# Kernel optimization log

Hardware: AMD Instinct MI355X
Metric: run time of the kernel (lower is better)

The kernel has to match this reference:

```python
import jax, jax.numpy as jnp
import numpy as np
from jax import lax

NAG = 3          # hardcoded in the torch module (query slices, catted_torches)
B = 4096         # batch_size per agent
H = 128          # hidden_dim
HEADS = 8
AD = H // HEADS  # attend_dim
STATE, ACT, SCAN = 48, 2, 256
OUTF, HID = 10, 256
NFEAT = 32 * (SCAN - 6)  # conv output features (two VALID convs: k5 then k3)
EPS = 1e-5

def leaky(x):
    return jnp.where(x >= 0, x, 0.01 * x)

def setup_inputs() -> dict:
    key = jax.random.key(0)
    ks = iter(jax.random.split(key, 40))
    def rn(shape, scale=0.05):
        return jax.random.normal(next(ks), shape, dtype=jnp.float32) * scale
    return {
        'obs':  jax.random.normal(next(ks), (NAG * B, STATE), jnp.float32),
        'acts': jax.random.normal(next(ks), (NAG * B, ACT), jnp.float32),
        'scan': jax.random.normal(next(ks), (NAG * B, SCAN), jnp.float32),
        'conv_w1': rn((32, 1, 5)),  'conv_b1': jnp.zeros((32,), jnp.float32),
        'conv_w2': rn((32, 32, 3)), 'conv_b2': jnp.zeros((32,), jnp.float32),
        'fc_w1': rn((256, NFEAT), 0.01), 'fc_b1': jnp.zeros((256,), jnp.float32),
        'fc_w2': rn((OUTF, 256)),        'fc_b2': jnp.zeros((OUTF,), jnp.float32),
        'enc_w': rn((H, STATE + ACT + OUTF)), 'enc_b': jnp.zeros((H,), jnp.float32),
        'Wk': rn((HEADS, AD, H)),
        'Wv': rn((HEADS, AD, H)), 'bv': jnp.zeros((HEADS, AD), jnp.float32),
        'Wq': rn((NAG, HEADS, AD, H)),
        'q1_w1': rn((HID, 2 * H)), 'q1_b1': jnp.zeros((HID,), jnp.float32),
        'q1_w2': rn((HID, HID)),   'q1_b2': jnp.zeros((HID,), jnp.float32),
        'q1_w3': rn((1, HID)),     'q1_b3': jnp.zeros((1,), jnp.float32),
        'q2_w1': rn((HID, 2 * H)), 'q2_b1': jnp.zeros((HID,), jnp.float32),
        'q2_w2': rn((HID, HID)),   'q2_b2': jnp.zeros((HID,), jnp.float32),
        'q2_w3': rn((1, HID)),     'q2_b3': jnp.zeros((1,), jnp.float32),
    }

def reference(obs, acts, scan, conv_w1, conv_b1, conv_w2, conv_b2,
              fc_w1, fc_b1, fc_w2, fc_b2, enc_w, enc_b, Wk, Wv, bv, Wq,
              q1_w1, q1_b1, q1_w2, q1_b2, q1_w3, q1_b3,
              q2_w1, q2_b1, q2_w2, q2_b2, q2_w3, q2_b3):
    dn = ('NCH', 'OIH', 'NCH')
    x = scan[:, None, :]                                            # [N,1,L]
    x = lax.conv_general_dilated(x, conv_w1, (1,), 'VALID', dimension_numbers=dn)
    x = jax.nn.relu(x + conv_b1[None, :, None])
    x = lax.conv_general_dilated(x, conv_w2, (1,), 'VALID', dimension_numbers=dn)
    x = jax.nn.relu(x + conv_b2[None, :, None])
    x = x.reshape(x.shape[0], -1)                                   # [N, NFEAT]
    x = jax.nn.relu(x @ fc_w1.T + fc_b1)
    feats = x @ fc_w2.T + fc_b2                                     # [N, OUTF]

    inps = jnp.concatenate([obs, acts, feats], axis=1)
    mu, var = inps.mean(0), inps.var(0)                             # BatchNorm1d (train, no affine)
    normed = (inps - mu) / jnp.sqrt(var + EPS)
    sa = leaky(normed @ enc_w.T + enc_b).reshape(NAG, B, H)         # [ag,B,H]

    keys = jnp.einsum('gbh,ndh->ngbd', sa, Wk)                      # [hd,ag,B,ad]
    vals = leaky(jnp.einsum('gbh,ndh->ngbd', sa, Wv) + bv[:, None, None, :])
    q = jnp.einsum('gbh,gndh->gnbd', sa, Wq)                        # [ag,hd,B,ad]

    logits = jnp.einsum('gnbd,nobd->gnbo', q, keys) / np.sqrt(AD)   # [ag,hd,B,ag]
    self_mask = jnp.eye(NAG, dtype=bool)[:, None, None, :]          # exclude own agent
    logits = jnp.where(self_mask, -jnp.inf, logits)
    w = jax.nn.softmax(logits, axis=-1)
    other = jnp.einsum('gnbo,nobd->gnbd', w, vals)                  # [ag,hd,B,ad]
    other = other.transpose(0, 2, 1, 3).reshape(NAG, B, H)          # heads concatenated

    emb = jnp.concatenate([sa, other], axis=2).reshape(NAG * B, 2 * H)

    def mlp(x, w1, b1, w2, b2, w3, b3):
        x = jax.nn.relu(x @ w1.T + b1)
        x = jax.nn.relu(x @ w2.T + b2)
        return x @ w3.T + b3

    q1 = mlp(emb, q1_w1, q1_b1, q1_w2, q1_b2, q1_w3, q1_b3)
    q2 = mlp(emb, q2_w1, q2_b1, q2_w2, q2_b2, q2_w3, q2_b3)
    return (q1, q2)
```

## Files before the change

### kernel.cpp

```cpp
#include <hip/hip_runtime.h>
#include <hip/hip_bf16.h>
#include <cstdint>
#include <cstddef>

typedef unsigned short u16;
typedef __attribute__((ext_vector_type(8))) __bf16 bf16x8;
typedef __attribute__((ext_vector_type(4))) float f32x4;

__device__ __forceinline__ u16 f2b(float f) {
  __hip_bfloat16 h = __float2bfloat16(f);
  return *reinterpret_cast<u16*>(&h);
}
__device__ __forceinline__ uint32_t pk2(float a, float b) {
  __hip_bfloat162 h = __float22bfloat162_rn(make_float2(a, b));
  return *reinterpret_cast<uint32_t*>(&h);
}
__device__ __forceinline__ float b2f(u16 u) {
  union { float f; uint32_t i; } x; x.i = ((uint32_t)u) << 16; return x.f;
}
__device__ __forceinline__ f32x4 mfma16(bf16x8 a, bf16x8 b, f32x4 c) {
  return __builtin_amdgcn_mfma_f32_16x16x32_bf16(a, b, c, 0, 0, 0);
}
__device__ __forceinline__ void async16(const void* g, void* l) {
  __builtin_amdgcn_global_load_lds((const __attribute__((address_space(1))) uint32_t*)g,
                                   (__attribute__((address_space(3))) uint32_t*)l, 16, 0, 0);
}

__global__ __launch_bounds__(256) void w1_perm(const float* __restrict__ w,
                                               u16* __restrict__ o) {
  __shared__ float L[8000];
  int j = blockIdx.x, tid = threadIdx.x;
  for (int i = tid; i < 8000; i += 256) L[i] = w[(size_t)j * 8000 + i];
  __syncthreads();
  for (int i = tid; i < 8000; i += 256) {
    int tt = i >> 5, cc = i & 31;
    int c2 = ((cc >> 2) & 1) * 16 + (cc >> 3) * 4 + (cc & 3);
    o[(size_t)j * 8000 + i] = f2b(L[c2 * 250 + tt]);
  }
}

struct CvtArgs {
  const float* src[13];
  void* dst[13];
  int cum[14];
  int kind[13];
};
__global__ __launch_bounds__(256) void f2b_multi(CvtArgs a, float* stats) {
  int i = blockIdx.x * 256 + threadIdx.x;
  if (blockIdx.x == 0 && threadIdx.x < 128) stats[threadIdx.x] = 0.f;
  int seg = 0;
  #pragma unroll
  for (int s = 1; s < 13; ++s) if (i >= a.cum[s]) seg = s;
  if (i < a.cum[13]) {
    int off = i - a.cum[seg];
    int kind = a.kind[seg];
    const float* src = a.src[seg];
    if (kind == 0) {
      ((u16*)a.dst[seg])[off] = f2b(src[off]);
    } else if (kind == 1) {
      int c2 = off / 96, rem = off - c2 * 96, kk = rem >> 5, c1 = rem & 31;
      ((u16*)a.dst[seg])[off] = f2b(src[(c2 * 32 + c1) * 3 + kk]);
    } else if (kind == 2) {
      int c1 = off >> 5, k = off & 31;
      ((u16*)a.dst[seg])[off] = f2b(k < 5 ? src[c1 * 5 + k] : 0.f);
    } else {
      ((float*)a.dst[seg])[off] = src[off];
    }
  }
}

__global__ __launch_bounds__(256) void conv_fused(
    const float* __restrict__ scan, const u16* __restrict__ w1g,
    const float* __restrict__ cb1, const u16* __restrict__ w2g,
    const float* __restrict__ cb2, u16* __restrict__ x) {
  __shared__ __align__(16) u16 A1[256 * 8];
  __shared__ __align__(16) u16 zbuf[4 * 8];
  __shared__ __align__(16) u16 h1T[258 * 40];
  int tid = threadIdx.x, lane = tid & 63, wv = tid >> 6;
  int l15 = lane & 15, quad = lane >> 4;
  const float* srow = scan + (size_t)blockIdx.x * 256;
  float sv[5];
  #pragma unroll
  for (int k = 0; k < 5; ++k) {
    int p = tid + k;
    sv[k] = (p < 256) ? srow[p] : 0.f;
  }
  union { bf16x8 v; uint32_t d[4]; } pk_;
  pk_.d[0] = pk2(sv[0], sv[1]);
  pk_.d[1] = pk2(sv[2], sv[3]);
  pk_.d[2] = pk2(sv[4], 0.f);
  pk_.d[3] = 0;
  *(bf16x8*)&A1[tid * 8] = pk_.v;
  if (lane < 8) zbuf[wv * 8 + lane] = 0;
  if (tid < 80) h1T[256 * 40 + tid] = 0;
  bf16x8 w1f[2];
  w1f[0] = *(const bf16x8*)&w1g[l15 * 32 + quad * 8];
  w1f[1] = *(const bf16x8*)&w1g[(16 + l15) * 32 + quad * 8];
  bf16x8 w2f[2][3];
  #pragma unroll
  for (int i = 0; i < 2; ++i)
    #pragma unroll
    for (int kk = 0; kk < 3; ++kk)
      w2f[i][kk] = *(const bf16x8*)&w2g[(i * 16 + l15) * 96 + kk * 32 + quad * 8];
  float cb1v[2][4], cb2v[2][4];
  #pragma unroll
  for (int i = 0; i < 2; ++i)
    #pragma unroll
    for (int r = 0; r < 4; ++r) {
      cb1v[i][r] = cb1[i * 16 + quad * 4 + r];
      cb2v[i][r] = cb2[i * 16 + quad * 4 + r];
    }
  asm volatile("s_waitcnt lgkmcnt(0)" ::: "memory");
  f32x4 zero = {0.f, 0.f, 0.f, 0.f};
  {
    f32x4 acc1[4][2];
    #pragma unroll
    for (int nt = 0; nt < 4; ++nt) { acc1[nt][0] = zero; acc1[nt][1] = zero; }
    #pragma unroll
    for (int nt = 0; nt < 4; ++nt) {
      int p = (wv * 4 + nt) * 16 + l15;
      const u16* bp = (quad == 0) ? &A1[p * 8] : &zbuf[wv * 8];
      bf16x8 bfr = *(const bf16x8*)bp;
      acc1[nt][0] = mfma16(w1f[0], bfr, acc1[nt][0]);
      acc1[nt][1] = mfma16(w1f[1], bfr, acc1[nt][1]);
    }
    #pragma unroll
    for (int nt = 0; nt < 4; ++nt) {
      int p = (wv * 4 + nt) * 16 + l15;
      #pragma unroll
      for (int mt = 0; mt < 2; ++mt) {
        float v0 = fmaxf(acc1[nt][mt][0] + cb1v[mt][0], 0.f);
        float v1 = fmaxf(acc1[nt][mt][1] + cb1v[mt][1], 0.f);
        float v2 = fmaxf(acc1[nt][mt][2] + cb1v[mt][2], 0.f);
        float v3 = fmaxf(acc1[nt][mt][3] + cb1v[mt][3], 0.f);
        uint2 u; u.x = pk2(v0, v1); u.y = pk2(v2, v3);
        *(uint2*)&h1T[p * 40 + mt * 16 + quad * 4] = u;
      }
    }
  }
  __syncthreads();
  f32x4 acc2[4][2];
  #pragma unroll
  for (int jj = 0; jj < 4; ++jj) { acc2[jj][0] = zero; acc2[jj][1] = zero; }
  #pragma unroll
  for (int kk = 0; kk < 3; ++kk) {
    #pragma unroll
    for (int jj = 0; jj < 4; ++jj) {
      int t = (wv * 4 + jj) * 16 + l15 + kk;
      bf16x8 h = *(const bf16x8*)&h1T[t * 40 + quad * 8];
      acc2[jj][0] = mfma16(w2f[0][kk], h, acc2[jj][0]);
      acc2[jj][1] = mfma16(w2f[1][kk], h, acc2[jj][1]);
    }
  }
  u16* xr = x + (size_t)blockIdx.x * 8000;
  #pragma unroll
  for (int jj = 0; jj < 4; ++jj) {
    int t = (wv * 4 + jj) * 16 + l15;
    if (t < 250) {
      union { bf16x8 v; uint32_t d[4]; } o_;
      #pragma unroll
      for (int i = 0; i < 2; ++i) {
        float v0 = fmaxf(acc2[jj][i][0] + cb2v[i][0], 0.f);
        float v1 = fmaxf(acc2[jj][i][1] + cb2v[i][1], 0.f);
        float v2 = fmaxf(acc2[jj][i][2] + cb2v[i][2], 0.f);
        float v3 = fmaxf(acc2[jj][i][3] + cb2v[i][3], 0.f);
        o_.d[i * 2]     = pk2(v0, v1);
        o_.d[i * 2 + 1] = pk2(v2, v3);
      }
      *(bf16x8*)&xr[t * 32 + quad * 8] = o_.v;
    }
  }
}

template <int MODE, int MROWS>
__global__ __launch_bounds__(256) void gemm_bt(
    const u16* __restrict__ A, int lda, const u16* __restrict__ W, int ldw,
    const float* __restrict__ bias, float* __restrict__ outF,
    u16* __restrict__ outB, int ldo, int nst, int a_sel, size_t out_zoff) {
  constexpr int AI = (MROWS * 8) / 256;
  __shared__ __align__(16) u16 As[2][MROWS * 64];
  __shared__ __align__(16) u16 Bs[2][128 * 64];
  int tid = threadIdx.x;
  int m0 = blockIdx.y * MROWS;
  int sel = (MODE == 4) ? blockIdx.x : 0;
  int n0 = (MODE == 4) ? 0 : blockIdx.x * 128;
  if (MODE == 4) {
    size_t woff = (sel < 2) ? (size_t)sel * 128 : (size_t)(256 + (m0 >> 12) * 128);
    W += woff * 128;
    outB += (size_t)sel * 12288 * 128;
  }
  if (a_sel) A += (size_t)(blockIdx.x >> 1) * a_sel;
  int kbase = blockIdx.z * nst * 64;
  if (MODE == 0) outF += (size_t)blockIdx.z * out_zoff;
  const u16* Ap = A + (size_t)m0 * lda + kbase;
  const u16* Wp = W + (size_t)n0 * ldw + kbase;
  int lane = tid & 63, wv = tid >> 6;
  int l15 = lane & 15, quad = lane >> 4;
  int wm = (wv >> 1) * (MROWS / 2), wn = (wv & 1) * 64;
  constexpr int MI = MROWS / 32;
  f32x4 zero = {0.f, 0.f, 0.f, 0.f};
  f32x4 acc[MI][4];
  #pragma unroll
  for (int i = 0; i < MI; ++i)
    #pragma unroll
    for (int j = 0; j < 4; ++j) acc[i][j] = zero;

  int sraA[AI], sofA[AI], sdsA[AI];
  #pragma unroll
  for (int it = 0; it < AI; ++it) {
    int c = it * 256 + tid;
    int row = c >> 3, slot = c & 7;
    sraA[it] = row;
    sofA[it] = ((slot ^ (row & 7)) * 8);
    sdsA[it] = c * 8;
  }
  int sraW[4], sofW[4], sdsW[4];
  #pragma unroll
  for (int it = 0; it < 4; ++it) {
    int c = it * 256 + tid;
    int row = c >> 3, slot = c & 7;
    sraW[it] = row;
    sofW[it] = ((slot ^ (row & 7)) * 8);
    sdsW[it] = c * 8;
  }
  int rslot[2];
  rslot[0] = ((quad ^ (l15 & 7)) * 8);
  rslot[1] = (((4 + quad) ^ (l15 & 7)) * 8);

  #pragma unroll 1
  for (int st = 0; st < nst; ++st) {
    if (st == 0) {
      #pragma unroll
      for (int it = 0; it < AI; ++it)
        async16(Ap + (size_t)sraA[it] * lda + sofA[it], &As[0][sdsA[it]]);
      #pragma unroll
      for (int it = 0; it < 4; ++it)
        async16(Wp + (size_t)sraW[it] * ldw + sofW[it], &Bs[0][sdsW[it]]);
    }
    __syncthreads();
    if (st + 1 < nst) {
      const u16* An = Ap + (st + 1) * 64;
      const u16* Wn = Wp + (st + 1) * 64;
      u16* Ad = &As[(st + 1) & 1][0];
      u16* Bd = &Bs[(st + 1) & 1][0];
      #pragma unroll
      for (int it = 0; it < AI; ++it)
        async16(An + (size_t)sraA[it] * lda + sofA[it], Ad + sdsA[it]);
      #pragma unroll
      for (int it = 0; it < 4; ++it)
        async16(Wn + (size_t)sraW[it] * ldw + sofW[it], Bd + sdsW[it]);
    }
    const u16* Ab = &As[st & 1][0];
    const u16* Bb = &Bs[st & 1][0];
    #pragma unroll
    for (int s = 0; s < 2; ++s) {
      bf16x8 af[MI], bfr[4];
      #pragma unroll
      for (int i = 0; i < MI; ++i)
        af[i] = *(const bf16x8*)&Ab[(wm + i * 16 + l15) * 64 + rslot[s]];
      #pragma unroll
      for (int j = 0; j < 4; ++j)
        bfr[j] = *(const bf16x8*)&Bb[(wn + j * 16 + l15) * 64 + rslot[s]];
      #pragma unroll
      for (int i = 0; i < MI; ++i)
        #pragma unroll
        for (int j = 0; j < 4; ++j) acc[i][j] = mfma16(af[i], bfr[j], acc[i][j]);
    }
  }
  #pragma unroll
  for (int i = 0; i < MI; ++i) {
    int mb = m0 + wm + i * 16 + quad * 4;
    #pragma unroll
    for (int j = 0; j < 4; ++j) {
      int n = n0 + wn + j * 16 + l15;
      float bv_ = (MODE == 1 || MODE == 4) ? bias[n] : 0.f;
      #pragma unroll
      for (int r = 0; r < 4; ++r) {
        float v = acc[i][j][r];
        if (MODE == 0) {
          outF[(size_t)(mb + r) * ldo + n] = v;
        } else if (MODE == 1) {
          v = fmaxf(v + bv_, 0.f);
          outB[(size_t)(mb + r) * ldo + n] = f2b(v);
        } else {
          if (sel == 1) { v += bv_; v = v >= 0.f ? v : 0.01f * v; }
          outB[(size_t)(mb + r) * ldo + n] = f2b(v);
        }
      }
    }
  }
}

__global__ __launch_bounds__(256) void fc2_stats(
    const float* __restrict__ hparts, const float* __restrict__ b1,
    const float* __restrict__ w2, const float* __restrict__ b2,
    const float* __restrict__ obs, const float* __restrict__ acts,
    float* __restrict__ inps, float* __restrict__ stats) {
  __shared__ float hL[32 * 260];
  __shared__ float w2L[10 * 260];
  __shared__ float b1L[256];
  __shared__ float ipL[32 * 61];
  int tid = threadIdx.x, r0 = blockIdx.x * 32;
  b1L[tid] = b1[tid];
  for (int i = tid; i < 2560; i += 256) w2L[(i >> 8) * 260 + (i & 255)] = w2[i];
  for (int i = tid; i < 32 * 48; i += 256) {
    int r = i / 48, f = i - r * 48;
    ipL[r * 61 + f] = obs[(size_t)(r0 + r) * 48 + f];
  }
  if (tid < 64) {
    int r = tid >> 1, f = tid & 1;
    ipL[r * 61 + 48 + f] = acts[(size_t)(r0 + r) * 2 + f];
  }
  __syncthreads();
  const size_t HS = (size_t)12288 * 256;
  for (int i = tid; i < 32 * 256; i += 256) {
    int r = i >> 8, c = i & 255;
    size_t g = (size_t)(r0 + r) * 256 + c;
    float v = b1L[c] + hparts[g] + hparts[g + HS] + hparts[g + 2 * HS] +
              hparts[g + 3 * HS] + hparts[g + 4 * HS];
    hL[r * 260 + c] = fmaxf(v, 0.f);
  }
  __syncthreads();
  {
    int r = tid >> 3, ob = tid & 7;
    for (int o = ob; o < 10; o += 8) {
      float a = 0.f;
      #pragma unroll 8
      for (int c = 0; c < 256; ++c) a += hL[r * 260 + c] * w2L[o * 260 + c];
      ipL[r * 61 + 50 + o] = a + b2[o];
    }
  }
  __syncthreads();
  for (int i = tid; i < 32 * 60; i += 256) {
    int r = i / 60, f = i - r * 60;
    inps[(size_t)(r0 + r) * 64 + f] = ipL[r * 61 + f];
  }
  if (tid < 60) {
    float s = 0.f, s2 = 0.f;
    for (int r = 0; r < 32; ++r) {
      float v = ipL[r * 61 + tid];
      s += v; s2 += v * v;
    }
    atomicAdd(&stats[tid], s);
    atomicAdd(&stats[64 + tid], s2);
  }
}

__global__ __launch_bounds__(256) void enc_kernel(
    const float* __restrict__ inps, const float* __restrict__ stats,
    const float* __restrict__ enc_w, const float* __restrict__ enc_b,
    u16* __restrict__ sab) {
  __shared__ float ewL[128 * 61];
  __shared__ float nrm[32 * 61];
  __shared__ float ebL[128];
  __shared__ float muL[60], ivL[60];
  int tid = threadIdx.x, r0 = blockIdx.x * 32;
  if (tid < 128) ebL[tid] = enc_b[tid];
  if (tid < 60) {
    float s = stats[tid], s2 = stats[64 + tid];
    float mu = s * (1.f / 12288.f);
    float var = s2 * (1.f / 12288.f) - mu * mu;
    muL[tid] = mu;
    ivL[tid] = rsqrtf(var + 1e-5f);
  }
  for (int i = tid; i < 128 * 60; i += 256) {
    int h = i / 60, f = i - h * 60;
    ewL[h * 61 + f] = enc_w[i];
  }
  __syncthreads();
  for (int i = tid; i < 32 * 60; i += 256) {
    int r = i / 60, f = i - r * 60;
    nrm[r * 61 + f] = (inps[(size_t)(r0 + r) * 64 + f] - muL[f]) * ivL[f];
  }
  __syncthreads();
  for (int i = tid; i < 32 * 128; i += 256) {
    int r = i >> 7, h = i & 127;
    float a = ebL[h];
    #pragma unroll 4
    for (int f = 0; f < 60; ++f) a += nrm[r * 61 + f] * ewL[h * 61 + f];
    a = a >= 0.f ? a : 0.01f * a;
    sab[(size_t)(r0 + r) * 128 + h] = f2b(a);
  }
}

__global__ __launch_bounds__(128) void attn_combine(
    const u16* __restrict__ qb, const u16* __restrict__ keysb,
    const u16* __restrict__ valsb, const u16* __restrict__ sab,
    u16* __restrict__ emb) {
  __shared__ float qL[3][128], kL[3][128], vL[3][128];
  __shared__ float lg[3][8][3], wgt[3][8][3];
  int b = blockIdx.x, t = threadIdx.x;
  #pragma unroll
  for (int o = 0; o < 3; ++o) {
    size_t base = (size_t)(o * 4096 + b) * 128 + t;
    qL[o][t] = b2f(qb[base]);
    kL[o][t] = b2f(keysb[base]);
    vL[o][t] = b2f(valsb[base]);
  }
  __syncthreads();
  if (t < 72) {
    int g = t / 24, n = (t / 3) % 8, o = t % 3;
    float a = 0.f;
    #pragma unroll
    for (int d = 0; d < 16; ++d) a += qL[g][n * 16 + d] * kL[o][n * 16 + d];
    lg[g][n][o] = (o == g) ? -1e30f : a * 0.25f;
  }
  __syncthreads();
  if (t < 24) {
    int g = t / 8, n = t % 8;
    float m = fmaxf(fmaxf(lg[g][n][0], lg[g][n][1]), lg[g][n][2]);
    float e0 = expf(lg[g][n][0] - m), e1 = expf(lg[g][n][1] - m),
          e2 = expf(lg[g][n][2] - m);
    float inv = 1.f / (e0 + e1 + e2);
    wgt[g][n][0] = e0 * inv; wgt[g][n][1] = e1 * inv; wgt[g][n][2] = e2 * inv;
  }
  __syncthreads();
  int n = t >> 4, d = t & 15;
  #pragma unroll
  for (int g = 0; g < 3; ++g) {
    float o_ = wgt[g][n][0] * vL[0][n * 16 + d] +
               wgt[g][n][1] * vL[1][n * 16 + d] +
               wgt[g][n][2] * vL[2][n * 16 + d];
    size_t rbase = (size_t)(g * 4096 + b) * 256;
    emb[rbase + 128 + t] = f2b(o_);
    emb[rbase + t] = sab[(size_t)(g * 4096 + b) * 128 + t];
  }
}

__global__ __launch_bounds__(256) void final_dot(
    const u16* __restrict__ t2ab, const float* __restrict__ w3a,
    const float* __restrict__ b3a, const float* __restrict__ w3b,
    const float* __restrict__ b3b, float* __restrict__ out) {
  int wv = threadIdx.x >> 6, lane = threadIdx.x & 63;
  int row = blockIdx.x * 4 + wv;
  float sa_ = 0.f, sb_ = 0.f;
  #pragma unroll
  for (int e = 0; e < 4; ++e) {
    int c = lane * 4 + e;
    sa_ += b2f(t2ab[(size_t)row * 512 + c]) * w3a[c];
    sb_ += b2f(t2ab[(size_t)row * 512 + 256 + c]) * w3b[c];
  }
  #pragma unroll
  for (int off = 32; off; off >>= 1) {
    sa_ += __shfl_down(sa_, off);
    sb_ += __shfl_down(sb_, off);
  }
  if (lane == 0) {
    out[row] = sa_ + b3a[0];
    out[12288 + row] = sb_ + b3b[0];
  }
}

extern "C" void kernel_launch(void* const* d_in, const int* in_sizes, int n_in,
                              void* d_out, int out_size, void* d_ws,
                              size_t ws_size, hipStream_t stream) {
  const float* obs  = (const float*)d_in[0];
  const float* acts = (const float*)d_in[1];
  const float* scan = (const float*)d_in[2];
  const float* cw1  = (const float*)d_in[3];
  const float* cb1  = (const float*)d_in[4];
  const float* cw2  = (const float*)d_in[5];
  const float* cb2  = (const float*)d_in[6];
  const float* fw1  = (const float*)d_in[7];
  const float* fb1  = (const float*)d_in[8];
  const float* fw2  = (const float*)d_in[9];
  const float* fb2  = (const float*)d_in[10];
  const float* encw = (const float*)d_in[11];
  const float* encb = (const float*)d_in[12];
  const float* Wk   = (const float*)d_in[13];
  const float* Wv   = (const float*)d_in[14];
  const float* bv   = (const float*)d_in[15];
  const float* Wq   = (const float*)d_in[16];
  const float* q1w1 = (const float*)d_in[17];
  const float* q1b1 = (const float*)d_in[18];
  const float* q1w2 = (const float*)d_in[19];
  const float* q1b2 = (const float*)d_in[20];
  const float* q1w3 = (const float*)d_in[21];
  const float* q1b3 = (const float*)d_in[22];
  const float* q2w1 = (const float*)d_in[23];
  const float* q2b1 = (const float*)d_in[24];
  const float* q2w2 = (const float*)d_in[25];
  const float* q2b2 = (const float*)d_in[26];
  const float* q2w3 = (const float*)d_in[27];
  const float* q2b3 = (const float*)d_in[28];
  float* out = (float*)d_out;
  char* ws = (char*)d_ws;
  if (ws_size < 264400000u) return;

  u16*   x     = (u16*)(ws + 0);
  u16*   w1b   = (u16*)(ws + 196608000);
  float* hpart = (float*)(ws + 200704000);
  float* stats = (float*)(ws + 263618560);
  u16*   wkvqb = (u16*)(ws + 263619584);
  u16*   m1ab  = (u16*)(ws + 263783424);
  u16*   m2ab  = (u16*)(ws + 264045568);
  u16*   w2g   = (u16*)(ws + 264307712);
  u16*   w1g   = (u16*)(ws + 264313856);
  float* bc1   = (float*)(ws + 264315904);
  float* bc2   = (float*)(ws + 264317952);
  float* inps  = (float*)(ws + 0);
  u16*   sab   = (u16*)(ws + 3145728);
  u16*   kvqb  = (u16*)(ws + 6291456);
  u16*   embb  = (u16*)(ws + 15728640);
  u16*   t1ab  = (u16*)(ws + 22020096);
  u16*   t2ab  = (u16*)(ws + 34603008);
  u16*   keysb = kvqb;
  u16*   valsb = kvqb + (size_t)12288 * 128;
  u16*   qb    = kvqb + (size_t)2 * 12288 * 128;

  w1_perm<<<256, 256, 0, stream>>>(fw1, w1b);
  CvtArgs ca;
  const float* srcs[13] = {Wk, Wv, Wq, q1w1, q2w1, q1w2, q2w2, cw2, cw1,
                           q1b1, q2b1, q1b2, q2b2};
  void* dsts[13] = {wkvqb, wkvqb + 16384, wkvqb + 32768, m1ab, m1ab + 65536,
                    m2ab, m2ab + 65536, w2g, w1g, bc1, bc1 + 256, bc2, bc2 + 256};
  const int sz[13] = {16384, 16384, 49152, 65536, 65536, 65536, 65536,
                      3072, 1024, 256, 256, 256, 256};
  const int kinds[13] = {0, 0, 0, 0, 0, 0, 0, 1, 2, 3, 3, 3, 3};
  int cum = 0;
  ca.cum[0] = 0;
  for (int i = 0; i < 13; ++i) {
    ca.src[i] = srcs[i]; ca.dst[i] = dsts[i]; ca.kind[i] = kinds[i];
    cum += sz[i]; ca.cum[i + 1] = cum;
  }
  f2b_multi<<<(cum + 255) / 256, 256, 0, stream>>>(ca, stats);

  conv_fused<<<12288, 256, 0, stream>>>(scan, w1g, cb1, w2g, cb2, x);
  gemm_bt<0, 64><<<dim3(2, 192, 5), 256, 0, stream>>>(
      x, 8000, w1b, 8000, nullptr, hpart, nullptr, 256, 25, 0,
      (size_t)12288 * 256);
  fc2_stats<<<384, 256, 0, stream>>>(hpart, fb1, fw2, fb2, obs, acts, inps, stats);
  enc_kernel<<<384, 256, 0, stream>>>(inps, stats, encw, encb, sab);
  gemm_bt<4, 64><<<dim3(3, 192, 1), 256, 0, stream>>>(
      sab, 128, wkvqb, 128, bv, nullptr, kvqb, 128, 2, 0, 0);
  attn_combine<<<4096, 128, 0, stream>>>(qb, keysb, valsb, sab, embb);
  gemm_bt<1, 64><<<dim3(4, 192, 1), 256, 0, stream>>>(
      embb, 256, m1ab, 256, bc1, nullptr, t1ab, 512, 4, 0, 0);
  gemm_bt<1, 64><<<dim3(4, 192, 1), 256, 0, stream>>>(
      t1ab, 512, m2ab, 256, bc2, nullptr, t2ab, 512, 4, 256, 0);
  final_dot<<<3072, 256, 0, stream>>>(t2ab, q1w3, q1b3, q2w3, q2b3, out);
}
```

Measured before the change: 364.3 us.

## Fuse conv stack into fc1 GEMM, streaming conv outputs through LDS

Replaces the separate conv kernel and split-K fc1 GEMM with one kernel. Each 512-thread block handles 64 rows: four waves compute the conv outputs one position at a time into a small LDS ring, and all eight waves consume them as K-slices of the fc1 GEMM, with double-buffered async weight loads. This removes the roughly 196MB bf16 intermediate and the split-K fp32 partial sums, and fc1 now writes a biased, ReLU'd bf16 output. The trade-off is only 192 blocks, a serial 250-step loop with a block barrier every step, and half the waves idle during the conv phase, so parallelism drops sharply.

Measured after the change: 430.5 us. 1.18x slower.

```diff
diff --git a/kernel.cpp b/kernel.cpp
--- a/kernel.cpp
+++ b/kernel.cpp
@@ -69,105 +69,176 @@
   }
 }
 
-__global__ __launch_bounds__(256) void conv_fused(
+__global__ __launch_bounds__(512) void mega(
     const float* __restrict__ scan, const u16* __restrict__ w1g,
     const float* __restrict__ cb1, const u16* __restrict__ w2g,
-    const float* __restrict__ cb2, u16* __restrict__ x) {
-  __shared__ __align__(16) u16 A1[256 * 8];
-  __shared__ __align__(16) u16 zbuf[4 * 8];
-  __shared__ __align__(16) u16 h1T[258 * 40];
+    const float* __restrict__ cb2, const u16* __restrict__ w1b,
+    const float* __restrict__ fb1, u16* __restrict__ hb) {
+  __shared__ __align__(16) u16 Ws[2][256 * 32];
+  __shared__ __align__(16) u16 Xs[2][64 * 40];
+  __shared__ __align__(16) u16 h1w[4][16 * 136];
   int tid = threadIdx.x, lane = tid & 63, wv = tid >> 6;
   int l15 = lane & 15, quad = lane >> 4;
-  const float* srow = scan + (size_t)blockIdx.x * 256;
-  float sv[5];
-  #pragma unroll
-  for (int k = 0; k < 5; ++k) {
-    int p = tid + k;
-    sv[k] = (p < 256) ? srow[p] : 0.f;
-  }
-  union { bf16x8 v; uint32_t d[4]; } pk_;
-  pk_.d[0] = pk2(sv[0], sv[1]);
-  pk_.d[1] = pk2(sv[2], sv[3]);
-  pk_.d[2] = pk2(sv[4], 0.f);
-  pk_.d[3] = 0;
-  *(bf16x8*)&A1[tid * 8] = pk_.v;
-  if (lane < 8) zbuf[wv * 8 + lane] = 0;
-  if (tid < 80) h1T[256 * 40 + tid] = 0;
-  bf16x8 w1f[2];
-  w1f[0] = *(const bf16x8*)&w1g[l15 * 32 + quad * 8];
-  w1f[1] = *(const bf16x8*)&w1g[(16 + l15) * 32 + quad * 8];
-  bf16x8 w2f[2][3];
-  #pragma unroll
-  for (int i = 0; i < 2; ++i)
-    #pragma unroll
-    for (int kk = 0; kk < 3; ++kk)
-      w2f[i][kk] = *(const bf16x8*)&w2g[(i * 16 + l15) * 96 + kk * 32 + quad * 8];
+  int r0 = blockIdx.x * 64;
+  f32x4 zero = {0.f, 0.f, 0.f, 0.f};
+  int wn = wv * 32;
+  f32x4 acc[4][2];
+  #pragma unroll
+  for (int i = 0; i < 4; ++i) { acc[i][0] = zero; acc[i][1] = zero; }
+  size_t wsrc[2]; int wdst[2];
+  #pragma unroll
+  for (int it = 0; it < 2; ++it) {
+    int c = it * 512 + tid;
+    int n = c >> 2, sl = c & 3;
+    int ks = sl ^ ((n >> 1) & 3);
+    wsrc[it] = (size_t)n * 8000 + ks * 8;
+    wdst[it] = c * 8;
+  }
+  int woff[2];
+  #pragma unroll
+  for (int j = 0; j < 2; ++j) {
+    int nj = wn + j * 16 + l15;
+    int sj = quad ^ ((nj >> 1) & 3);
+    woff[j] = nj * 32 + sj * 8;
+  }
+  int xoff[4];
+  #pragma unroll
+  for (int i = 0; i < 4; ++i) xoff[i] = (i * 16 + l15) * 40 + quad * 8;
+
+  bool cw = wv < 4;
+  const float* srow = scan + (size_t)(r0 + (wv & 3) * 16 + l15) * 256;
+  u16* myh1 = &h1w[wv & 3][0];
+  int h1wo = l15 * 136 + quad * 4;
+  int h1ro = l15 * 136 + quad * 8;
+  int xwo = ((wv & 3) * 16 + l15) * 40 + quad * 8;
+  bf16x8 w1f[2], w2f[2][3];
   float cb1v[2][4], cb2v[2][4];
-  #pragma unroll
-  for (int i = 0; i < 2; ++i)
-    #pragma unroll
-    for (int r = 0; r < 4; ++r) {
-      cb1v[i][r] = cb1[i * 16 + quad * 4 + r];
-      cb2v[i][r] = cb2[i * 16 + quad * 4 + r];
-    }
-  asm volatile("s_waitcnt lgkmcnt(0)" ::: "memory");
-  f32x4 zero = {0.f, 0.f, 0.f, 0.f};
-  {
-    f32x4 acc1[4][2];
-    #pragma unroll
-    for (int nt = 0; nt < 4; ++nt) { acc1[nt][0] = zero; acc1[nt][1] = zero; }
-    #pragma unroll
-    for (int nt = 0; nt < 4; ++nt) {
-      int p = (wv * 4 + nt) * 16 + l15;
-      const u16* bp = (quad == 0) ? &A1[p * 8] : &zbuf[wv * 8];
-      bf16x8 bfr = *(const bf16x8*)bp;
-      acc1[nt][0] = mfma16(w1f[0], bfr, acc1[nt][0]);
-      acc1[nt][1] = mfma16(w1f[1], bfr, acc1[nt][1]);
-    }
-    #pragma unroll
-    for (int nt = 0; nt < 4; ++nt) {
-      int p = (wv * 4 + nt) * 16 + l15;
-      #pragma unroll
-      for (int mt = 0; mt < 2; ++mt) {
-        float v0 = fmaxf(acc1[nt][mt][0] + cb1v[mt][0], 0.f);
-        float v1 = fmaxf(acc1[nt][mt][1] + cb1v[mt][1], 0.f);
-        float v2 = fmaxf(acc1[nt][mt][2] + cb1v[mt][2], 0.f);
-        float v3 = fmaxf(acc1[nt][mt][3] + cb1v[mt][3], 0.f);
-        uint2 u; u.x = pk2(v0, v1); u.y = pk2(v2, v3);
-        *(uint2*)&h1T[p * 40 + mt * 16 + quad * 4] = u;
+  if (cw) {
+    w1f[0] = *(const bf16x8*)&w1g[l15 * 32 + quad * 8];
+    w1f[1] = *(const bf16x8*)&w1g[(16 + l15) * 32 + quad * 8];
+    #pragma unroll
+    for (int i = 0; i < 2; ++i)
+      #pragma unroll
+      for (int kk = 0; kk < 3; ++kk)
+        w2f[i][kk] = *(const bf16x8*)&w2g[(i * 16 + l15) * 96 + kk * 32 + quad * 8];
+    #pragma unroll
+    for (int i = 0; i < 2; ++i)
+      #pragma unroll
+      for (int r = 0; r < 4; ++r) {
+        cb1v[i][r] = cb1[i * 16 + quad * 4 + r];
+        cb2v[i][r] = cb2[i * 16 + quad * 4 + r];
       }
-    }
-  }
-  __syncthreads();
-  f32x4 acc2[4][2];
-  #pragma unroll
-  for (int jj = 0; jj < 4; ++jj) { acc2[jj][0] = zero; acc2[jj][1] = zero; }
-  #pragma unroll
-  for (int kk = 0; kk < 3; ++kk) {
-    #pragma unroll
-    for (int jj = 0; jj < 4; ++jj) {
-      int t = (wv * 4 + jj) * 16 + l15 + kk;
-      bf16x8 h = *(const bf16x8*)&h1T[t * 40 + quad * 8];
-      acc2[jj][0] = mfma16(w2f[0][kk], h, acc2[jj][0]);
-      acc2[jj][1] = mfma16(w2f[1][kk], h, acc2[jj][1]);
-    }
-  }
-  u16* xr = x + (size_t)blockIdx.x * 8000;
-  #pragma unroll
-  for (int jj = 0; jj < 4; ++jj) {
-    int t = (wv * 4 + jj) * 16 + l15;
-    if (t < 250) {
-      union { bf16x8 v; uint32_t d[4]; } o_;
-      #pragma unroll
-      for (int i = 0; i < 2; ++i) {
-        float v0 = fmaxf(acc2[jj][i][0] + cb2v[i][0], 0.f);
-        float v1 = fmaxf(acc2[jj][i][1] + cb2v[i][1], 0.f);
-        float v2 = fmaxf(acc2[jj][i][2] + cb2v[i][2], 0.f);
-        float v3 = fmaxf(acc2[jj][i][3] + cb2v[i][3], 0.f);
-        o_.d[i * 2]     = pk2(v0, v1);
-        o_.d[i * 2 + 1] = pk2(v2, v3);
+  }
+  float sreg[5] = {0.f, 0.f, 0.f, 0.f, 0.f};
+
+  auto conv1_step = [&](int slot) {
+    union { bf16x8 v; uint32_t d[4]; } u;
+    uint32_t d0 = pk2(sreg[0], sreg[1]);
+    uint32_t d1 = pk2(sreg[2], sreg[3]);
+    uint32_t d2 = pk2(sreg[4], 0.f);
+    u.d[0] = (quad == 0) ? d0 : 0u;
+    u.d[1] = (quad == 0) ? d1 : 0u;
+    u.d[2] = (quad == 0) ? d2 : 0u;
+    u.d[3] = 0u;
+    f32x4 a0 = mfma16(w1f[0], u.v, zero);
+    f32x4 a1 = mfma16(w1f[1], u.v, zero);
+    #pragma unroll
+    for (int mt = 0; mt < 2; ++mt) {
+      f32x4 a = mt ? a1 : a0;
+      float v0 = fmaxf(a[0] + cb1v[mt][0], 0.f);
+      float v1 = fmaxf(a[1] + cb1v[mt][1], 0.f);
+      float v2 = fmaxf(a[2] + cb1v[mt][2], 0.f);
+      float v3 = fmaxf(a[3] + cb1v[mt][3], 0.f);
+      uint2 w; w.x = pk2(v0, v1); w.y = pk2(v2, v3);
+      *(uint2*)&myh1[h1wo + slot * 32 + mt * 16] = w;
+    }
+  };
+
+  #pragma unroll
+  for (int it = 0; it < 2; ++it)
+    async16(w1b + wsrc[it], &Ws[0][wdst[it]]);
+  if (cw) {
+    if (quad == 0) {
+      #pragma unroll
+      for (int k = 0; k < 5; ++k) sreg[k] = srow[k];
+    }
+    conv1_step(0);
+    if (quad == 0) {
+      sreg[0] = sreg[1]; sreg[1] = sreg[2]; sreg[2] = sreg[3]; sreg[3] = sreg[4];
+      sreg[4] = srow[5];
+    }
+    conv1_step(1);
+    if (quad == 0) {
+      sreg[0] = sreg[1]; sreg[1] = sreg[2]; sreg[2] = sreg[3]; sreg[3] = sreg[4];
+      sreg[4] = srow[6];
+    }
+  }
+
+  #pragma unroll 1
+  for (int t = 0; t < 250; ++t) {
+    int buf = t & 1;
+    if (cw) {
+      conv1_step((t + 2) & 3);
+      if (quad == 0) {
+        sreg[0] = sreg[1]; sreg[1] = sreg[2]; sreg[2] = sreg[3]; sreg[3] = sreg[4];
+        if (t < 249) sreg[4] = srow[t + 7];
       }
-      *(bf16x8*)&xr[t * 32 + quad * 8] = o_.v;
+      f32x4 c0 = zero, c1 = zero;
+      #pragma unroll
+      for (int kk = 0; kk < 3; ++kk) {
+        int slot = (t + kk) & 3;
+        bf16x8 h = *(const bf16x8*)&myh1[h1ro + slot * 32];
+        c0 = mfma16(w2f[0][kk], h, c0);
+        c1 = mfma16(w2f[1][kk], h, c1);
+      }
+      union { bf16x8 v; uint32_t d[4]; } o;
+      {
+        float v0 = fmaxf(c0[0] + cb2v[0][0], 0.f);
+        float v1 = fmaxf(c0[1] + cb2v[0][1], 0.f);
+        float v2 = fmaxf(c0[2] + cb2v[0][2], 0.f);
+        float v3 = fmaxf(c0[3] + cb2v[0][3], 0.f);
+        o.d[0] = pk2(v0, v1); o.d[1] = pk2(v2, v3);
+        float w0 = fmaxf(c1[0] + cb2v[1][0], 0.f);
+        float w1 = fmaxf(c1[1] + cb2v[1][1], 0.f);
+        float w2 = fmaxf(c1[2] + cb2v[1][2], 0.f);
+        float w3 = fmaxf(c1[3] + cb2v[1][3], 0.f);
+        o.d[2] = pk2(w0, w1); o.d[3] = pk2(w2, w3);
+      }
+      *(bf16x8*)&Xs[buf][xwo] = o.v;
+    }
+    __syncthreads();
+    if (t < 249) {
+      int kb = (t + 1) * 32;
+      u16* Wd = &Ws[(t + 1) & 1][0];
+      #pragma unroll
+      for (int it = 0; it < 2; ++it)
+        async16(w1b + wsrc[it] + kb, Wd + wdst[it]);
+    }
+    const u16* Wb = &Ws[buf][0];
+    const u16* Xb = &Xs[buf][0];
+    bf16x8 bw0 = *(const bf16x8*)&Wb[woff[0]];
+    bf16x8 bw1 = *(const bf16x8*)&Wb[woff[1]];
+    #pragma unroll
+    for (int i = 0; i < 4; ++i) {
+      bf16x8 bx = *(const bf16x8*)&Xb[xoff[i]];
+      acc[i][0] = mfma16(bx, bw0, acc[i][0]);
+      acc[i][1] = mfma16(bx, bw1, acc[i][1]);
+    }
+  }
+  float b1v[2];
+  b1v[0] = fb1[wn + l15];
+  b1v[1] = fb1[wn + 16 + l15];
+  #pragma unroll
+  for (int i = 0; i < 4; ++i) {
+    int row = r0 + i * 16 + quad * 4;
+    #pragma unroll
+    for (int j = 0; j < 2; ++j) {
+      int n = wn + j * 16 + l15;
+      #pragma unroll
+      for (int r = 0; r < 4; ++r) {
+        float v = fmaxf(acc[i][j][r] + b1v[j], 0.f);
+        hb[(size_t)(row + r) * 256 + n] = f2b(v);
+      }
     }
   }
 }
@@ -292,16 +363,14 @@
 }
 
 __global__ __launch_bounds__(256) void fc2_stats(
-    const float* __restrict__ hparts, const float* __restrict__ b1,
-    const float* __restrict__ w2, const float* __restrict__ b2,
-    const float* __restrict__ obs, const float* __restrict__ acts,
-    float* __restrict__ inps, float* __restrict__ stats) {
+    const u16* __restrict__ hb, const float* __restrict__ w2,
+    const float* __restrict__ b2, const float* __restrict__ obs,
+    const float* __restrict__ acts, float* __restrict__ inps,
+    float* __restrict__ stats) {
   __shared__ float hL[32 * 260];
   __shared__ float w2L[10 * 260];
-  __shared__ float b1L[256];
   __shared__ float ipL[32 * 61];
   int tid = threadIdx.x, r0 = blockIdx.x * 32;
-  b1L[tid] = b1[tid];
   for (int i = tid; i < 2560; i += 256) w2L[(i >> 8) * 260 + (i & 255)] = w2[i];
   for (int i = tid; i < 32 * 48; i += 256) {
     int r = i / 48, f = i - r * 48;
@@ -311,14 +380,11 @@
     int r = tid >> 1, f = tid & 1;
     ipL[r * 61 + 48 + f] = acts[(size_t)(r0 + r) * 2 + f];
   }
-  __syncthreads();
-  const size_t HS = (size_t)12288 * 256;
-  for (int i = tid; i < 32 * 256; i += 256) {
-    int r = i >> 8, c = i & 255;
-    size_t g = (size_t)(r0 + r) * 256 + c;
-    float v = b1L[c] + hparts[g] + hparts[g + HS] + hparts[g + 2 * HS] +
-              hparts[g + 3 * HS] + hparts[g + 4 * HS];
-    hL[r * 260 + c] = fmaxf(v, 0.f);
+  for (int i = tid; i < 1024; i += 256) {
+    int r = i >> 5, cv = (i & 31) * 8;
+    const u16* hp = &hb[(size_t)(r0 + r) * 256 + cv];
+    #pragma unroll
+    for (int e = 0; e < 8; ++e) hL[r * 260 + cv + e] = b2f(hp[e]);
   }
   __syncthreads();
   {
@@ -485,25 +551,24 @@
   const float* q2b3 = (const float*)d_in[28];
   float* out = (float*)d_out;
   char* ws = (char*)d_ws;
-  if (ws_size < 264400000u) return;
-
-  u16*   x     = (u16*)(ws + 0);
-  u16*   w1b   = (u16*)(ws + 196608000);
-  float* hpart = (float*)(ws + 200704000);
-  float* stats = (float*)(ws + 263618560);
-  u16*   wkvqb = (u16*)(ws + 263619584);
-  u16*   m1ab  = (u16*)(ws + 263783424);
-  u16*   m2ab  = (u16*)(ws + 264045568);
-  u16*   w2g   = (u16*)(ws + 264307712);
-  u16*   w1g   = (u16*)(ws + 264313856);
-  float* bc1   = (float*)(ws + 264315904);
-  float* bc2   = (float*)(ws + 264317952);
-  float* inps  = (float*)(ws + 0);
-  u16*   sab   = (u16*)(ws + 3145728);
-  u16*   kvqb  = (u16*)(ws + 6291456);
-  u16*   embb  = (u16*)(ws + 15728640);
-  u16*   t1ab  = (u16*)(ws + 22020096);
-  u16*   t2ab  = (u16*)(ws + 34603008);
+  if (ws_size < 60000000u) return;
+
+  u16*   hb    = (u16*)(ws + 0);
+  float* inps  = (float*)(ws + 6291456);
+  u16*   sab   = (u16*)(ws + 9437184);
+  u16*   kvqb  = (u16*)(ws + 12582912);
+  u16*   embb  = (u16*)(ws + 22020096);
+  u16*   t1ab  = (u16*)(ws + 28311552);
+  u16*   t2ab  = (u16*)(ws + 40894464);
+  u16*   w1b   = (u16*)(ws + 53477376);
+  float* stats = (float*)(ws + 57573376);
+  u16*   wkvqb = (u16*)(ws + 57574400);
+  u16*   m1ab  = (u16*)(ws + 57738240);
+  u16*   m2ab  = (u16*)(ws + 58000384);
+  u16*   w2g   = (u16*)(ws + 58262528);
+  u16*   w1g   = (u16*)(ws + 58268672);
+  float* bc1   = (float*)(ws + 58270720);
+  float* bc2   = (float*)(ws + 58272768);
   u16*   keysb = kvqb;
   u16*   valsb = kvqb + (size_t)12288 * 128;
   u16*   qb    = kvqb + (size_t)2 * 12288 * 128;
@@ -525,11 +590,8 @@
   }
   f2b_multi<<<(cum + 255) / 256, 256, 0, stream>>>(ca, stats);
 
-  conv_fused<<<12288, 256, 0, stream>>>(scan, w1g, cb1, w2g, cb2, x);
-  gemm_bt<0, 64><<<dim3(2, 192, 5), 256, 0, stream>>>(
-      x, 8000, w1b, 8000, nullptr, hpart, nullptr, 256, 25, 0,
-      (size_t)12288 * 256);
-  fc2_stats<<<384, 256, 0, stream>>>(hpart, fb1, fw2, fb2, obs, acts, inps, stats);
+  mega<<<192, 512, 0, stream>>>(scan, w1g, cb1, w2g, cb2, w1b, fb1, hb);
+  fc2_stats<<<384, 256, 0, stream>>>(hb, fw2, fb2, obs, acts, inps, stats);
   enc_kernel<<<384, 256, 0, stream>>>(inps, stats, encw, encb, sab);
   gemm_bt<4, 64><<<dim3(3, 192, 1), 256, 0, stream>>>(
       sab, 128, wkvqb, 128, bv, nullptr, kvqb, 128, 2, 0, 0);
```

## Fuse final MLP dot into second MLP GEMM epilogue; enlarge fc1 GEMM tile

Applied to the files above, without the earlier changes.

The second hidden-layer GEMM now applies bias and ReLU, multiplies by the output-layer weights and reduces across columns in registers. It writes per-block partial dot products instead of a bf16 activation tensor, and a small kernel sums the partials and adds the output bias. This removes the write and re-read of the 12288x512 activation and the separate final_dot pass. Separately, the large fc1 GEMM switches from 64-row to 128-row tiles to improve weight reuse, at the cost of fewer blocks and more registers or shared memory per block.

New measurement: 364.7 us (median of 2 runs). No clear change (+0.1%).

```diff
diff --git a/kernel.cpp b/kernel.cpp
--- a/kernel.cpp
+++ b/kernel.cpp
@@ -40,18 +40,18 @@
 }
 
 struct CvtArgs {
-  const float* src[13];
-  void* dst[13];
-  int cum[14];
-  int kind[13];
+  const float* src[15];
+  void* dst[15];
+  int cum[16];
+  int kind[15];
 };
 __global__ __launch_bounds__(256) void f2b_multi(CvtArgs a, float* stats) {
   int i = blockIdx.x * 256 + threadIdx.x;
   if (blockIdx.x == 0 && threadIdx.x < 128) stats[threadIdx.x] = 0.f;
   int seg = 0;
   #pragma unroll
-  for (int s = 1; s < 13; ++s) if (i >= a.cum[s]) seg = s;
-  if (i < a.cum[13]) {
+  for (int s = 1; s < 15; ++s) if (i >= a.cum[s]) seg = s;
+  if (i < a.cum[15]) {
     int off = i - a.cum[seg];
     int kind = a.kind[seg];
     const float* src = a.src[seg];
@@ -176,7 +176,8 @@
 __global__ __launch_bounds__(256) void gemm_bt(
     const u16* __restrict__ A, int lda, const u16* __restrict__ W, int ldw,
     const float* __restrict__ bias, float* __restrict__ outF,
-    u16* __restrict__ outB, int ldo, int nst, int a_sel, size_t out_zoff) {
+    u16* __restrict__ outB, int ldo, int nst, int a_sel, size_t out_zoff,
+    const float* __restrict__ w3cat, float* __restrict__ pd) {
   constexpr int AI = (MROWS * 8) / 256;
   __shared__ __align__(16) u16 As[2][MROWS * 64];
   __shared__ __align__(16) u16 Bs[2][128 * 64];
@@ -266,6 +267,35 @@
         #pragma unroll
         for (int j = 0; j < 4; ++j) acc[i][j] = mfma16(af[i], bfr[j], acc[i][j]);
     }
+  }
+  if (MODE == 5) {
+    float w3v[4], bv4[4];
+    #pragma unroll
+    for (int j = 0; j < 4; ++j) {
+      int n = n0 + wn + j * 16 + l15;
+      w3v[j] = w3cat[n];
+      bv4[j] = bias[n];
+    }
+    int sblk = (n0 >> 7) * 2 + (wv & 1);
+    #pragma unroll
+    for (int i = 0; i < MI; ++i) {
+      int mb = m0 + wm + i * 16 + quad * 4;
+      #pragma unroll
+      for (int r = 0; r < 4; ++r) {
+        float s = 0.f;
+        #pragma unroll
+        for (int j = 0; j < 4; ++j) {
+          float v = fmaxf(acc[i][j][r] + bv4[j], 0.f);
+          s += v * w3v[j];
+        }
+        s += __shfl_down(s, 8);
+        s += __shfl_down(s, 4);
+        s += __shfl_down(s, 2);
+        s += __shfl_down(s, 1);
+        if (l15 == 0) pd[(size_t)sblk * 12288 + mb + r] = s;
+      }
+    }
+    return;
   }
   #pragma unroll
   for (int i = 0; i < MI; ++i) {
@@ -427,28 +457,15 @@
   }
 }
 
-__global__ __launch_bounds__(256) void final_dot(
-    const u16* __restrict__ t2ab, const float* __restrict__ w3a,
-    const float* __restrict__ b3a, const float* __restrict__ w3b,
+__global__ __launch_bounds__(256) void final_sum(
+    const float* __restrict__ pd, const float* __restrict__ b3a,
     const float* __restrict__ b3b, float* __restrict__ out) {
-  int wv = threadIdx.x >> 6, lane = threadIdx.x & 63;
-  int row = blockIdx.x * 4 + wv;
-  float sa_ = 0.f, sb_ = 0.f;
-  #pragma unroll
-  for (int e = 0; e < 4; ++e) {
-    int c = lane * 4 + e;
-    sa_ += b2f(t2ab[(size_t)row * 512 + c]) * w3a[c];
-    sb_ += b2f(t2ab[(size_t)row * 512 + 256 + c]) * w3b[c];
-  }
-  #pragma unroll
-  for (int off = 32; off; off >>= 1) {
-    sa_ += __shfl_down(sa_, off);
-    sb_ += __shfl_down(sb_, off);
-  }
-  if (lane == 0) {
-    out[row] = sa_ + b3a[0];
-    out[12288 + row] = sb_ + b3b[0];
-  }
+  int row = blockIdx.x * 256 + threadIdx.x;
+  const size_t R = 12288;
+  float s1 = pd[row] + pd[R + row] + pd[2 * R + row] + pd[3 * R + row];
+  float s2 = pd[4 * R + row] + pd[5 * R + row] + pd[6 * R + row] + pd[7 * R + row];
+  out[row] = s1 + b3a[0];
+  out[R + row] = s2 + b3b[0];
 }
 
 extern "C" void kernel_launch(void* const* d_in, const int* in_sizes, int n_in,
@@ -498,45 +515,47 @@
   u16*   w1g   = (u16*)(ws + 264313856);
   float* bc1   = (float*)(ws + 264315904);
   float* bc2   = (float*)(ws + 264317952);
+  float* w3cat = (float*)(ws + 264320000);
   float* inps  = (float*)(ws + 0);
   u16*   sab   = (u16*)(ws + 3145728);
   u16*   kvqb  = (u16*)(ws + 6291456);
   u16*   embb  = (u16*)(ws + 15728640);
   u16*   t1ab  = (u16*)(ws + 22020096);
-  u16*   t2ab  = (u16*)(ws + 34603008);
+  float* pd    = (float*)(ws + 34603008);
   u16*   keysb = kvqb;
   u16*   valsb = kvqb + (size_t)12288 * 128;
   u16*   qb    = kvqb + (size_t)2 * 12288 * 128;
 
   w1_perm<<<256, 256, 0, stream>>>(fw1, w1b);
   CvtArgs ca;
-  const float* srcs[13] = {Wk, Wv, Wq, q1w1, q2w1, q1w2, q2w2, cw2, cw1,
-                           q1b1, q2b1, q1b2, q2b2};
-  void* dsts[13] = {wkvqb, wkvqb + 16384, wkvqb + 32768, m1ab, m1ab + 65536,
-                    m2ab, m2ab + 65536, w2g, w1g, bc1, bc1 + 256, bc2, bc2 + 256};
-  const int sz[13] = {16384, 16384, 49152, 65536, 65536, 65536, 65536,
-                      3072, 1024, 256, 256, 256, 256};
-  const int kinds[13] = {0, 0, 0, 0, 0, 0, 0, 1, 2, 3, 3, 3, 3};
+  const float* srcs[15] = {Wk, Wv, Wq, q1w1, q2w1, q1w2, q2w2, cw2, cw1,
+                           q1b1, q2b1, q1b2, q2b2, q1w3, q2w3};
+  void* dsts[15] = {wkvqb, wkvqb + 16384, wkvqb + 32768, m1ab, m1ab + 65536,
+                    m2ab, m2ab + 65536, w2g, w1g, bc1, bc1 + 256, bc2,
+                    bc2 + 256, w3cat, w3cat + 256};
+  const int sz[15] = {16384, 16384, 49152, 65536, 65536, 65536, 65536,
+                      3072, 1024, 256, 256, 256, 256, 256, 256};
+  const int kinds[15] = {0, 0, 0, 0, 0, 0, 0, 1, 2, 3, 3, 3, 3, 3, 3};
   int cum = 0;
   ca.cum[0] = 0;
-  for (int i = 0; i < 13; ++i) {
+  for (int i = 0; i < 15; ++i) {
     ca.src[i] = srcs[i]; ca.dst[i] = dsts[i]; ca.kind[i] = kinds[i];
     cum += sz[i]; ca.cum[i + 1] = cum;
   }
   f2b_multi<<<(cum + 255) / 256, 256, 0, stream>>>(ca, stats);
 
   conv_fused<<<12288, 256, 0, stream>>>(scan, w1g, cb1, w2g, cb2, x);
-  gemm_bt<0, 64><<<dim3(2, 192, 5), 256, 0, stream>>>(
+  gemm_bt<0, 128><<<dim3(2, 96, 5), 256, 0, stream>>>(
       x, 8000, w1b, 8000, nullptr, hpart, nullptr, 256, 25, 0,
-      (size_t)12288 * 256);
+      (size_t)12288 * 256, nullptr, nullptr);
   fc2_stats<<<384, 256, 0, stream>>>(hpart, fb1, fw2, fb2, obs, acts, inps, stats);
   enc_kernel<<<384, 256, 0, stream>>>(inps, stats, encw, encb, sab);
   gemm_bt<4, 64><<<dim3(3, 192, 1), 256, 0, stream>>>(
-      sab, 128, wkvqb, 128, bv, nullptr, kvqb, 128, 2, 0, 0);
+      sab, 128, wkvqb, 128, bv, nullptr, kvqb, 128, 2, 0, 0, nullptr, nullptr);
   attn_combine<<<4096, 128, 0, stream>>>(qb, keysb, valsb, sab, embb);
   gemm_bt<1, 64><<<dim3(4, 192, 1), 256, 0, stream>>>(
-      embb, 256, m1ab, 256, bc1, nullptr, t1ab, 512, 4, 0, 0);
-  gemm_bt<1, 64><<<dim3(4, 192, 1), 256, 0, stream>>>(
-      t1ab, 512, m2ab, 256, bc2, nullptr, t2ab, 512, 4, 256, 0);
-  final_dot<<<3072, 256, 0, stream>>>(t2ab, q1w3, q1b3, q2w3, q2b3, out);
-}
+      embb, 256, m1ab, 256, bc1, nullptr, t1ab, 512, 4, 0, 0, nullptr, nullptr);
+  gemm_bt<5, 64><<<dim3(4, 192, 1), 256, 0, stream>>>(
+      t1ab, 512, m2ab, 256, bc2, nullptr, nullptr, 0, 4, 256, 0, w3cat, pd);
+  final_sum<<<48, 256, 0, stream>>>(pd, q1b3, q2b3, out);
+}
```
